# Optimization experiments

Hardware: AMD Instinct MI355X
Metric: run time of the kernel (lower is better)

Reference implementation:

```python
import jax, jax.numpy as jnp
import numpy as np

DIM = 2048
STATE = 16
BATCH = 2
SEQ = 2048
LN_EPS = 1e-5


def setup_inputs() -> dict:
    key = jax.random.key(0)
    ks = jax.random.split(key, 12)
    d, n = DIM, STATE
    inp = {
        "x": jax.random.normal(ks[0], (BATCH, SEQ, d), dtype=jnp.float32),
        "ln_gamma": jnp.ones((d,), dtype=jnp.float32),
        "ln_beta": jnp.zeros((d,), dtype=jnp.float32),
        # proj_in: Linear(d, 2d) (spectral-normed; weights treated as effective)
        "W_in": jax.random.normal(ks[1], (2 * d, d), dtype=jnp.float32) / np.sqrt(d),
        "b_in": jnp.zeros((2 * d,), dtype=jnp.float32),
        "state_A": jax.random.normal(ks[2], (n, d), dtype=jnp.float32) * 0.01,
        "W_B": jax.random.normal(ks[3], (n, d), dtype=jnp.float32) / np.sqrt(d),
        "b_B": jnp.zeros((n,), dtype=jnp.float32),
        "W_C": jax.random.normal(ks[4], (n, d), dtype=jnp.float32) / np.sqrt(d),
        "b_C": jnp.zeros((n,), dtype=jnp.float32),
        "W_dt": jax.random.normal(ks[5], (d, d), dtype=jnp.float32) / np.sqrt(d),
        "b_dt": jnp.zeros((d,), dtype=jnp.float32),
        "W_out": jax.random.normal(ks[6], (d, d), dtype=jnp.float32) / np.sqrt(d),
        "b_out": jnp.zeros((d,), dtype=jnp.float32),
    }
    return inp


def reference(x, ln_gamma, ln_beta, W_in, b_in, state_A, W_B, b_B, W_C, b_C,
              W_dt, b_dt, W_out, b_out):
    residual = x
    # LayerNorm over last dim
    mu = jnp.mean(x, axis=-1, keepdims=True)
    var = jnp.mean(jnp.square(x - mu), axis=-1, keepdims=True)
    xn = (x - mu) * jax.lax.rsqrt(var + LN_EPS) * ln_gamma + ln_beta
    # input projection and gate split
    xz = jnp.einsum('bsd,ed->bse', xn, W_in) + b_in          # (B,S,2D)
    x_ssm, z = jnp.split(xz, 2, axis=-1)                      # (B,S,D) each
    # dt = clamp(softplus(proj_dt(x_ssm)), max=1.0)
    dt = jnp.minimum(jax.nn.softplus(jnp.einsum('bsd,ed->bse', x_ssm, W_dt) + b_dt), 1.0)
    Bm = jnp.einsum('bsd,nd->bsn', x_ssm, W_B) + b_B          # (B,S,N)
    Cm = jnp.einsum('bsd,nd->bsn', x_ssm, W_C) + b_C          # (B,S,N)
    # A_bar[b,s,n,d] = exp(state_A[n,d] * dt[b,s,d])
    A_bar = jnp.exp(state_A[None, None, :, :] * dt[:, :, None, :])  # (B,S,N,D)
    # y[b,s,d] = sum_n C[b,s,n]*B[b,s,n]*A_bar[b,s,n,d] * x_ssm[b,s,d]
    y = jnp.einsum('bsn,bsnd->bsd', Cm * Bm, A_bar) * x_ssm
    gated = y * jax.nn.silu(z)
    out = jnp.einsum('bsd,ed->bse', gated, W_out) + b_out
    return out + residual
```

## Files before the change

kernel.cpp:

```cpp
#include <hip/hip_runtime.h>

typedef unsigned short u16;
typedef float f32x4 __attribute__((ext_vector_type(4)));
typedef __bf16 bf16x8 __attribute__((ext_vector_type(8)));

__device__ __forceinline__ u16 f2bf(float f) {
    unsigned u = __float_as_uint(f);
    u += 0x7FFFu + ((u >> 16) & 1u);
    return (u16)(u >> 16);
}
__device__ __forceinline__ float b2f(u16 h) {
    return __uint_as_float(((unsigned)h) << 16);
}

__device__ __forceinline__ void async16(const u16* g, u16* l) {
    __builtin_amdgcn_global_load_lds(
        (__attribute__((address_space(1))) void*)(u16*)g,
        (__attribute__((address_space(3))) void*)l,
        16, 0, 0);
}

#define T_TOK 4096
#define DIM   2048

__global__ __launch_bounds__(256) void castln_kernel(const float* __restrict__ W_in,
                                                     u16* __restrict__ wb_in,
                                                     const float* __restrict__ x,
                                                     const float* __restrict__ g,
                                                     const float* __restrict__ b,
                                                     u16* __restrict__ o) {
    __shared__ float s1[4], s2[4];
    int blk = blockIdx.x, tid = threadIdx.x;
    if (blk < 8192) {
        int i = blk * 256 + tid;
        float4 f = ((const float4*)W_in)[i];
        ushort4 u;
        u.x = f2bf(f.x); u.y = f2bf(f.y); u.z = f2bf(f.z); u.w = f2bf(f.w);
        ((ushort4*)wb_in)[i] = u;
        return;
    }
    int t = blk - 8192;
    int wave = tid >> 6, lane = tid & 63;
    size_t base = (size_t)t * DIM;
    int d0 = tid * 8;
    float4 v0 = *(const float4*)(x + base + d0);
    float4 v1 = *(const float4*)(x + base + d0 + 4);
    float v[8] = {v0.x, v0.y, v0.z, v0.w, v1.x, v1.y, v1.z, v1.w};
    float s = 0.f;
#pragma unroll
    for (int j = 0; j < 8; ++j) s += v[j];
#pragma unroll
    for (int o2 = 32; o2; o2 >>= 1) s += __shfl_xor(s, o2);
    if (lane == 0) s1[wave] = s;
    __syncthreads();
    float mu = (s1[0] + s1[1] + s1[2] + s1[3]) * (1.f / DIM);
    float q = 0.f;
#pragma unroll
    for (int j = 0; j < 8; ++j) { float dd = v[j] - mu; q += dd * dd; }
#pragma unroll
    for (int o2 = 32; o2; o2 >>= 1) q += __shfl_xor(q, o2);
    if (lane == 0) s2[wave] = q;
    __syncthreads();
    float var = (s2[0] + s2[1] + s2[2] + s2[3]) * (1.f / DIM);
    float rs = rsqrtf(var + 1e-5f);
    float4 g0 = *(const float4*)(g + d0), g1 = *(const float4*)(g + d0 + 4);
    float4 b0 = *(const float4*)(b + d0), b1 = *(const float4*)(b + d0 + 4);
    float gv[8] = {g0.x, g0.y, g0.z, g0.w, g1.x, g1.y, g1.z, g1.w};
    float bv[8] = {b0.x, b0.y, b0.z, b0.w, b1.x, b1.y, b1.z, b1.w};
    ushort4 r0, r1;
    u16* rp0 = (u16*)&r0; u16* rp1 = (u16*)&r1;
#pragma unroll
    for (int j = 0; j < 4; ++j) {
        rp0[j] = f2bf((v[j] - mu) * rs * gv[j] + bv[j]);
        rp1[j] = f2bf((v[j + 4] - mu) * rs * gv[j + 4] + bv[j + 4]);
    }
    *(ushort4*)(o + base + d0) = r0;
    *(ushort4*)(o + base + d0 + 4) = r1;
}

__global__ __launch_bounds__(256) void cast4_kernel(const float* __restrict__ s0, u16* __restrict__ d0, int n0,
                                                    const float* __restrict__ s1, u16* __restrict__ d1, int n1,
                                                    const float* __restrict__ s2, u16* __restrict__ d2, int n2,
                                                    const float* __restrict__ s3, u16* __restrict__ d3, int n3) {
    int j = blockIdx.x * 256 + threadIdx.x;
    const float* s; u16* d;
    if (j < n0) { s = s0; d = d0; }
    else {
        j -= n0;
        if (j < n1) { s = s1; d = d1; }
        else {
            j -= n1;
            if (j < n2) { s = s2; d = d2; }
            else { j -= n2; if (j >= n3) return; s = s3; d = d3; }
        }
    }
    float4 f = ((const float4*)s)[j];
    ushort4 u;
    u.x = f2bf(f.x); u.y = f2bf(f.y); u.z = f2bf(f.z); u.w = f2bf(f.w);
    ((ushort4*)d)[j] = u;
}

#define WBM 128
#define WBN 128
#define WBK 64

__global__ __launch_bounds__(256) void gemm_wide(const u16* __restrict__ A,
                                                 const u16* __restrict__ W,
                                                 const float* __restrict__ bias,
                                                 u16* __restrict__ Xs,
                                                 u16* __restrict__ Z, int K) {
    __shared__ __align__(16) u16 lAB[(WBM + WBN) * WBK];
    const int tid = threadIdx.x;
    const int wave = tid >> 6, lane = tid & 63;
    const int quad = lane >> 4, l16 = lane & 15;
    const int tM = blockIdx.x * WBM;
    const int tN = blockIdx.y * WBN;
    const int wr = wave >> 1, wc = wave & 1;

    const int rowin = tid >> 3;
    const int col8 = ((tid & 7) ^ (rowin & 7)) * 8;
    const u16* gptr[8];
    u16* ldst[8];
#pragma unroll
    for (int i = 0; i < 8; ++i) {
        int trow = i * 32 + rowin;
        const u16* src = (i < 4) ? (A + (size_t)(tM + trow) * 2048)
                                 : (W + (size_t)(tN + (trow - WBM)) * 2048);
        gptr[i] = src + col8;
        ldst[i] = &lAB[(i * 32 + wave * 8) * WBK];
    }

    int a_off[2][4], b_off[2][4];
#pragma unroll
    for (int h = 0; h < 2; ++h) {
#pragma unroll
        for (int mi = 0; mi < 4; ++mi)
            a_off[h][mi] = (wr * 64 + mi * 16 + l16) * WBK +
                           (((h * 4 + quad) ^ (l16 & 7)) * 8);
#pragma unroll
        for (int ni = 0; ni < 4; ++ni)
            b_off[h][ni] = (WBM + wc * 64 + ni * 16 + l16) * WBK +
                           (((h * 4 + quad) ^ (l16 & 7)) * 8);
    }

    f32x4 acc[4][4] = {};

    for (int kt = 0; kt < K; kt += WBK) {
#pragma unroll
        for (int i = 0; i < 8; ++i) async16(gptr[i] + kt, ldst[i]);
        __syncthreads();
#pragma unroll
        for (int h = 0; h < 2; ++h) {
            bf16x8 af[4], bfr[4];
#pragma unroll
            for (int i = 0; i < 4; ++i) af[i] = *(const bf16x8*)&lAB[a_off[h][i]];
#pragma unroll
            for (int i = 0; i < 4; ++i) bfr[i] = *(const bf16x8*)&lAB[b_off[h][i]];
#pragma unroll
            for (int mi = 0; mi < 4; ++mi)
#pragma unroll
                for (int ni = 0; ni < 4; ++ni)
                    acc[mi][ni] = __builtin_amdgcn_mfma_f32_16x16x32_bf16(
                        af[mi], bfr[ni], acc[mi][ni], 0, 0, 0);
        }
        __syncthreads();
    }

    const bool isb_z = (tN >= 2048);
    u16* dst = isb_z ? Z : Xs;
#pragma unroll
    for (int mi = 0; mi < 4; ++mi) {
#pragma unroll
        for (int ni = 0; ni < 4; ++ni) {
            int col = tN + wc * 64 + ni * 16 + l16;
            float bv = bias[col];
            int ocol = isb_z ? (col - 2048) : col;
#pragma unroll
            for (int r = 0; r < 4; ++r) {
                int row = tM + wr * 64 + mi * 16 + quad * 4 + r;
                dst[(size_t)row * 2048 + ocol] = f2bf(acc[mi][ni][r] + bv);
            }
        }
    }
}

#define NBM 128
#define NBN 64
#define NBK 64

template <int EPI>
__global__ __launch_bounds__(256) void gemm_nw(const u16* __restrict__ A, int lda,
                                               const u16* __restrict__ W, int ldw,
                                               const float* __restrict__ bias,
                                               const float* __restrict__ resid,
                                               void* __restrict__ C, int ldc, int K,
                                               u16* __restrict__ dots) {
    __shared__ __align__(16) u16 lAB[(NBM + NBN) * NBK];
    const int tid = threadIdx.x;
    const int wave = tid >> 6, lane = tid & 63;
    const int quad = lane >> 4, l16 = lane & 15;
    const int tM = blockIdx.x * NBM;
    const int tN = blockIdx.y * NBN;
    const int wr = wave >> 1, wc = wave & 1;

    const int rowin = tid >> 3;
    const int r3 = rowin & 7;
    const int col8 = ((tid & 7) ^ r3) * 8;
    const u16* gptr[6];
    u16* ldst[6];
#pragma unroll
    for (int i = 0; i < 6; ++i) {
        int trow = i * 32 + rowin;
        const u16* src = (i < 4) ? (A + (size_t)(tM + trow) * lda)
                                 : (W + (size_t)(tN + (trow - NBM)) * ldw);
        gptr[i] = src + col8;
        ldst[i] = &lAB[(i * 32 + wave * 8) * NBK];
    }

    int a_off[2][4], b_off[2][2];
#pragma unroll
    for (int h = 0; h < 2; ++h) {
#pragma unroll
        for (int mi = 0; mi < 4; ++mi)
            a_off[h][mi] = (wr * 64 + mi * 16 + l16) * NBK +
                           (((h * 4 + quad) ^ (l16 & 7)) * 8);
#pragma unroll
        for (int ni = 0; ni < 2; ++ni)
            b_off[h][ni] = (NBM + wc * 32 + ni * 16 + l16) * NBK +
                           (((h * 4 + quad) ^ (l16 & 7)) * 8);
    }

    f32x4 acc[4][2] = {};

    for (int kt = 0; kt < K; kt += NBK) {
#pragma unroll
        for (int i = 0; i < 6; ++i) async16(gptr[i] + kt, ldst[i]);
        __syncthreads();
        bf16x8 af[2][4], bfr[2][2];
#pragma unroll
        for (int h = 0; h < 2; ++h) {
#pragma unroll
            for (int mi = 0; mi < 4; ++mi) af[h][mi] = *(const bf16x8*)&lAB[a_off[h][mi]];
#pragma unroll
            for (int ni = 0; ni < 2; ++ni) bfr[h][ni] = *(const bf16x8*)&lAB[b_off[h][ni]];
        }
#pragma unroll
        for (int h = 0; h < 2; ++h)
#pragma unroll
            for (int mi = 0; mi < 4; ++mi)
#pragma unroll
                for (int ni = 0; ni < 2; ++ni)
                    acc[mi][ni] = __builtin_amdgcn_mfma_f32_16x16x32_bf16(
                        af[h][mi], bfr[h][ni], acc[mi][ni], 0, 0, 0);
        __syncthreads();
    }

#pragma unroll
    for (int mi = 0; mi < 4; ++mi) {
#pragma unroll
        for (int ni = 0; ni < 2; ++ni) {
            int col = tN + wc * 32 + ni * 16 + l16;
            float bv = (EPI == 1 && col >= 2048) ? 0.f : bias[col];
#pragma unroll
            for (int r = 0; r < 4; ++r) {
                int row = tM + wr * 64 + mi * 16 + quad * 4 + r;
                float v = acc[mi][ni][r] + bv;
                if constexpr (EPI == 1) {
                    if (col < 2048) {
                        float sp = (v > 20.f) ? v : log1pf(__expf(v));
                        ((u16*)C)[(size_t)row * ldc + col] = f2bf(fminf(sp, 1.0f));
                    } else if (col < 2080) {
                        dots[(size_t)row * 32 + (col - 2048)] = f2bf(v);
                    }
                } else {
                    size_t idx = (size_t)row * ldc + col;
                    ((float*)C)[idx] = v + resid[idx];
                }
            }
        }
    }
}

__global__ __launch_bounds__(256) void ssm_gate_kernel(const u16* __restrict__ dtb,
                                                       const u16* __restrict__ xsb,
                                                       const u16* __restrict__ zb,
                                                       const float* __restrict__ A,
                                                       const u16* __restrict__ dots,
                                                       const float* __restrict__ bB,
                                                       const float* __restrict__ bC,
                                                       u16* __restrict__ gated) {
    __shared__ float Pl[16];
    int t = blockIdx.x, tid = threadIdx.x;
    if (tid < 16) {
        float Bv = b2f(dots[(size_t)t * 32 + tid]) + bB[tid];
        float Cv = b2f(dots[(size_t)t * 32 + 16 + tid]) + bC[tid];
        Pl[tid] = Bv * Cv;
    }
    __syncthreads();
    size_t dbase = (size_t)t * DIM;
    int d0 = tid * 8;
    ushort4 dth[2], xsh[2], zh[2];
    dth[0] = *(const ushort4*)(dtb + dbase + d0);
    dth[1] = *(const ushort4*)(dtb + dbase + d0 + 4);
    xsh[0] = *(const ushort4*)(xsb + dbase + d0);
    xsh[1] = *(const ushort4*)(xsb + dbase + d0 + 4);
    zh[0]  = *(const ushort4*)(zb + dbase + d0);
    zh[1]  = *(const ushort4*)(zb + dbase + d0 + 4);
    float dtv[8], xsv[8], zv[8];
#pragma unroll
    for (int h = 0; h < 2; ++h) {
        const u16* dp = (const u16*)&dth[h];
        const u16* xp = (const u16*)&xsh[h];
        const u16* zp = (const u16*)&zh[h];
#pragma unroll
        for (int j = 0; j < 4; ++j) {
            dtv[h * 4 + j] = b2f(dp[j]);
            xsv[h * 4 + j] = b2f(xp[j]);
            zv[h * 4 + j]  = b2f(zp[j]);
        }
    }
    float s[8] = {};
#pragma unroll
    for (int n = 0; n < 16; ++n) {
        float4 a0 = *(const float4*)(A + n * DIM + d0);
        float4 a1 = *(const float4*)(A + n * DIM + d0 + 4);
        float pn = Pl[n];
        float av[8] = {a0.x, a0.y, a0.z, a0.w, a1.x, a1.y, a1.z, a1.w};
#pragma unroll
        for (int j = 0; j < 8; ++j) s[j] += pn * __expf(av[j] * dtv[j]);
    }
    ushort4 r0, r1;
    u16* rp0 = (u16*)&r0; u16* rp1 = (u16*)&r1;
#pragma unroll
    for (int j = 0; j < 8; ++j) {
        float y = s[j] * xsv[j];
        float sz = zv[j] * (1.0f / (1.0f + __expf(-zv[j])));
        u16 hv = f2bf(y * sz);
        if (j < 4) rp0[j] = hv; else rp1[j - 4] = hv;
    }
    *(ushort4*)(gated + dbase + d0) = r0;
    *(ushort4*)(gated + dbase + d0 + 4) = r1;
}

extern "C" void kernel_launch(void* const* d_in, const int* in_sizes, int n_in,
                              void* d_out, int out_size, void* d_ws, size_t ws_size,
                              hipStream_t stream) {
    const float* x      = (const float*)d_in[0];
    const float* ln_g   = (const float*)d_in[1];
    const float* ln_b   = (const float*)d_in[2];
    const float* W_in   = (const float*)d_in[3];
    const float* b_in   = (const float*)d_in[4];
    const float* stateA = (const float*)d_in[5];
    const float* W_B    = (const float*)d_in[6];
    const float* b_B    = (const float*)d_in[7];
    const float* W_C    = (const float*)d_in[8];
    const float* b_C    = (const float*)d_in[9];
    const float* W_dt   = (const float*)d_in[10];
    const float* b_dt   = (const float*)d_in[11];
    const float* W_out  = (const float*)d_in[12];
    const float* b_out  = (const float*)d_in[13];

    char* ws = (char*)d_ws;
    u16*   wb_in  = (u16*)(ws);
    u16*   wb_out = (u16*)(ws);
    u16*   xnb    = (u16*)(ws + 16777216);
    u16*   wb_dt  = (u16*)(ws + 16777216);
    u16*   gated  = (u16*)(ws + 16777216);
    u16*   xsb    = (u16*)(ws + 33554432);
    u16*   zb     = (u16*)(ws + 50331648);
    u16*   dtb    = (u16*)(ws + 67108864);
    u16*   dotsb  = (u16*)(ws + 83886080);

    castln_kernel<<<12288, 256, 0, stream>>>(W_in, wb_in, x, ln_g, ln_b, xnb);
    gemm_wide<<<dim3(32, 32), 256, 0, stream>>>(xnb, wb_in, b_in, xsb, zb, 2048);
    cast4_kernel<<<8256, 256, 0, stream>>>(
        W_dt, wb_dt, 1048576,
        W_B,  wb_dt + (size_t)2048 * 2048, 8192,
        W_C,  wb_dt + (size_t)2064 * 2048, 8192,
        W_out, wb_out, 1048576);
    gemm_nw<1><<<dim3(32, 33), 256, 0, stream>>>(xsb, 2048, wb_dt, 2048, b_dt,
                                                 nullptr, dtb, 2048, 2048, dotsb);
    ssm_gate_kernel<<<T_TOK, 256, 0, stream>>>(dtb, xsb, zb, stateA, dotsb,
                                               b_B, b_C, gated);
    gemm_nw<2><<<dim3(32, 32), 256, 0, stream>>>(gated, 2048, wb_out, 2048, b_out,
                                                 x, (float*)d_out, 2048, 2048, nullptr);
}
```

Before: 405.0 us.

## Rewrite wide input GEMM as 256x256 double-buffered pipelined kernel with 8 waves

The input-projection GEMM moves from 128x128 tiles with 4 waves and a single LDS buffer to 256x256 tiles with 8 waves, double-buffered LDS, and async global-to-LDS staging spread across eight compute phases. Explicit vmcnt waits, scheduling barriers and setprio are meant to overlap memory loads with MFMA work, while the larger tile improves data reuse. The cost is 128KB of LDS per block and only 256 blocks, so occupancy is low and the kernel depends on the hand-written schedule being correct.

```diff
diff --git a/kernel.cpp b/kernel.cpp
--- a/kernel.cpp
+++ b/kernel.cpp
@@ -100,76 +100,120 @@
     ((ushort4*)d)[j] = u;
 }
 
-#define WBM 128
-#define WBN 128
-#define WBK 64
-
-__global__ __launch_bounds__(256) void gemm_wide(const u16* __restrict__ A,
+#define GBM 256
+#define GBN 256
+#define GBK 64
+
+#define WAITV4 asm volatile("s_waitcnt vmcnt(4)" ::: "memory")
+#define SBAR() do { __builtin_amdgcn_sched_barrier(0); __builtin_amdgcn_s_barrier(); } while (0)
+
+__global__ __launch_bounds__(512) void gemm_wide(const u16* __restrict__ A,
                                                  const u16* __restrict__ W,
                                                  const float* __restrict__ bias,
                                                  u16* __restrict__ Xs,
                                                  u16* __restrict__ Z, int K) {
-    __shared__ __align__(16) u16 lAB[(WBM + WBN) * WBK];
+    __shared__ __align__(16) u16 lA[2][GBM * GBK];
+    __shared__ __align__(16) u16 lB[2][GBN * GBK];
     const int tid = threadIdx.x;
-    const int wave = tid >> 6, lane = tid & 63;
+    const int wv = tid >> 6, lane = tid & 63;
     const int quad = lane >> 4, l16 = lane & 15;
-    const int tM = blockIdx.x * WBM;
-    const int tN = blockIdx.y * WBN;
-    const int wr = wave >> 1, wc = wave & 1;
-
-    const int rowin = tid >> 3;
-    const int col8 = ((tid & 7) ^ (rowin & 7)) * 8;
-    const u16* gptr[8];
-    u16* ldst[8];
-#pragma unroll
-    for (int i = 0; i < 8; ++i) {
-        int trow = i * 32 + rowin;
-        const u16* src = (i < 4) ? (A + (size_t)(tM + trow) * 2048)
-                                 : (W + (size_t)(tN + (trow - WBM)) * 2048);
-        gptr[i] = src + col8;
-        ldst[i] = &lAB[(i * 32 + wave * 8) * WBK];
-    }
-
-    int a_off[2][4], b_off[2][4];
-#pragma unroll
-    for (int h = 0; h < 2; ++h) {
+    const int wr = wv >> 2, wc = wv & 3;
+    const int tM = blockIdx.x * GBM, tN = blockIdx.y * GBN;
+
+    const int srow = tid >> 3;
+    const int swz = ((tid & 7) ^ (srow & 7)) * 8;
+    const u16* gA = A + (size_t)(tM + srow) * 2048 + swz;
+    const u16* gW = W + (size_t)(tN + srow) * 2048 + swz;
+
+#define STAGE_A(BI, KC) do {                                                  \
+    _Pragma("unroll") for (int r_ = 0; r_ < 4; ++r_)                          \
+      async16(gA + (size_t)r_ * 64 * 2048 + (KC),                             \
+              &lA[BI][(r_ * 64 + wv * 8) * GBK]);                             \
+  } while (0)
+#define STAGE_B(BI, KC) do {                                                  \
+    _Pragma("unroll") for (int r_ = 0; r_ < 4; ++r_)                          \
+      async16(gW + (size_t)r_ * 64 * 2048 + (KC),                             \
+              &lB[BI][(r_ * 64 + wv * 8) * GBK]);                             \
+  } while (0)
+
+    int aoff[2][4][2], boff[2][2][2];
+#pragma unroll
+    for (int qm = 0; qm < 2; ++qm)
 #pragma unroll
         for (int mi = 0; mi < 4; ++mi)
-            a_off[h][mi] = (wr * 64 + mi * 16 + l16) * WBK +
-                           (((h * 4 + quad) ^ (l16 & 7)) * 8);
-#pragma unroll
-        for (int ni = 0; ni < 4; ++ni)
-            b_off[h][ni] = (WBM + wc * 64 + ni * 16 + l16) * WBK +
-                           (((h * 4 + quad) ^ (l16 & 7)) * 8);
-    }
-
-    f32x4 acc[4][4] = {};
-
-    for (int kt = 0; kt < K; kt += WBK) {
-#pragma unroll
-        for (int i = 0; i < 8; ++i) async16(gptr[i] + kt, ldst[i]);
-        __syncthreads();
-#pragma unroll
-        for (int h = 0; h < 2; ++h) {
-            bf16x8 af[4], bfr[4];
-#pragma unroll
-            for (int i = 0; i < 4; ++i) af[i] = *(const bf16x8*)&lAB[a_off[h][i]];
-#pragma unroll
-            for (int i = 0; i < 4; ++i) bfr[i] = *(const bf16x8*)&lAB[b_off[h][i]];
-#pragma unroll
-            for (int mi = 0; mi < 4; ++mi)
-#pragma unroll
-                for (int ni = 0; ni < 4; ++ni)
-                    acc[mi][ni] = __builtin_amdgcn_mfma_f32_16x16x32_bf16(
-                        af[mi], bfr[ni], acc[mi][ni], 0, 0, 0);
-        }
-        __syncthreads();
-    }
+#pragma unroll
+            for (int h = 0; h < 2; ++h) {
+                int row = wr * 128 + (qm * 4 + mi) * 16 + l16;
+                aoff[qm][mi][h] = row * GBK + (((h * 4 + quad) ^ (l16 & 7)) * 8);
+            }
+#pragma unroll
+    for (int qn = 0; qn < 2; ++qn)
+#pragma unroll
+        for (int ni = 0; ni < 2; ++ni)
+#pragma unroll
+            for (int h = 0; h < 2; ++h) {
+                int row = wc * 64 + (qn * 2 + ni) * 16 + l16;
+                boff[qn][ni][h] = row * GBK + (((h * 4 + quad) ^ (l16 & 7)) * 8);
+            }
+
+    f32x4 acc[8][4] = {};
+    bf16x8 af[4][2];
+
+#define PHASE(BI, QM, QN, LOADA, STAGE_STMT, WAIT_STMT) do {                  \
+    if (LOADA) {                                                              \
+      _Pragma("unroll") for (int mi_ = 0; mi_ < 4; ++mi_)                     \
+        _Pragma("unroll") for (int h_ = 0; h_ < 2; ++h_)                      \
+          af[mi_][h_] = *(const bf16x8*)&lA[BI][aoff[QM][mi_][h_]];           \
+    }                                                                         \
+    bf16x8 bfr_[2][2];                                                        \
+    _Pragma("unroll") for (int ni_ = 0; ni_ < 2; ++ni_)                       \
+      _Pragma("unroll") for (int h_ = 0; h_ < 2; ++h_)                        \
+        bfr_[ni_][h_] = *(const bf16x8*)&lB[BI][boff[QN][ni_][h_]];           \
+    STAGE_STMT;                                                               \
+    SBAR();                                                                   \
+    __builtin_amdgcn_s_setprio(1);                                            \
+    _Pragma("unroll") for (int mi_ = 0; mi_ < 4; ++mi_)                       \
+      _Pragma("unroll") for (int ni_ = 0; ni_ < 2; ++ni_)                     \
+        _Pragma("unroll") for (int h_ = 0; h_ < 2; ++h_)                      \
+          acc[QM * 4 + mi_][QN * 2 + ni_] =                                   \
+              __builtin_amdgcn_mfma_f32_16x16x32_bf16(                        \
+                  af[mi_][h_], bfr_[ni_][h_],                                 \
+                  acc[QM * 4 + mi_][QN * 2 + ni_], 0, 0, 0);                  \
+    __builtin_amdgcn_s_setprio(0);                                            \
+    WAIT_STMT;                                                                \
+    SBAR();                                                                   \
+  } while (0)
+
+    STAGE_A(0, 0);
+    STAGE_B(0, 0);
+    STAGE_A(1, 64);
+    WAITV4;
+    SBAR();
+
+    const int NIT = K >> 7;
+    for (int it = 0; it < NIT; ++it) {
+        const int k1 = it * 128 + 64;
+        int kn = it * 128 + 128;
+        if (kn > K - 64) kn = K - 64;
+        int kn1 = it * 128 + 192;
+        if (kn1 > K - 64) kn1 = K - 64;
+
+        PHASE(0, 0, 0, 1, STAGE_B(1, k1), (void)0);
+        PHASE(0, 0, 1, 0, (void)0,        (void)0);
+        PHASE(0, 1, 0, 1, (void)0,        (void)0);
+        PHASE(0, 1, 1, 0, STAGE_A(0, kn), WAITV4);
+        PHASE(1, 0, 0, 1, STAGE_B(0, kn), (void)0);
+        PHASE(1, 0, 1, 0, (void)0,        (void)0);
+        PHASE(1, 1, 0, 1, (void)0,        (void)0);
+        PHASE(1, 1, 1, 0, STAGE_A(1, kn1), WAITV4);
+    }
+
+    asm volatile("s_waitcnt vmcnt(0)" ::: "memory");
 
     const bool isb_z = (tN >= 2048);
     u16* dst = isb_z ? Z : Xs;
 #pragma unroll
-    for (int mi = 0; mi < 4; ++mi) {
+    for (int mi = 0; mi < 8; ++mi) {
 #pragma unroll
         for (int ni = 0; ni < 4; ++ni) {
             int col = tN + wc * 64 + ni * 16 + l16;
@@ -177,11 +221,14 @@
             int ocol = isb_z ? (col - 2048) : col;
 #pragma unroll
             for (int r = 0; r < 4; ++r) {
-                int row = tM + wr * 64 + mi * 16 + quad * 4 + r;
+                int row = tM + wr * 128 + mi * 16 + quad * 4 + r;
                 dst[(size_t)row * 2048 + ocol] = f2bf(acc[mi][ni][r] + bv);
             }
         }
     }
+#undef PHASE
+#undef STAGE_A
+#undef STAGE_B
 }
 
 #define NBM 128
@@ -372,7 +419,7 @@
     u16*   dotsb  = (u16*)(ws + 83886080);
 
     castln_kernel<<<12288, 256, 0, stream>>>(W_in, wb_in, x, ln_g, ln_b, xnb);
-    gemm_wide<<<dim3(32, 32), 256, 0, stream>>>(xnb, wb_in, b_in, xsb, zb, 2048);
+    gemm_wide<<<dim3(16, 16), 512, 0, stream>>>(xnb, wb_in, b_in, xsb, zb, 2048);
     cast4_kernel<<<8256, 256, 0, stream>>>(
         W_dt, wb_dt, 1048576,
         W_B,  wb_dt + (size_t)2048 * 2048, 8192,
```

After: 385.6 us. -4.8%, faster.
